# Optimization experiments

Measured on AMD Instinct MI355X. Metric: run time of the kernel, lower is better.

## Reference

```python
import jax, jax.numpy as jnp
import numpy as np

B, S, D, H = 2, 2048, 768, 12
HD = D // H


def setup_inputs() -> dict:
    key = jax.random.key(0)
    ks = jax.random.split(key, 6)
    x = jax.random.normal(ks[0], (B, S, D), dtype=jnp.float32)
    # causal mask: 1.0 where attention is disallowed (upper triangle), broadcast to [B,H,S,S]
    mask = (1.0 - jnp.tril(jnp.ones((S, S), dtype=jnp.float32)))[None, None]
    std = 0.02
    Wq = jax.random.normal(ks[1], (D, D), dtype=jnp.float32) * std
    Wk = jax.random.normal(ks[2], (D, D), dtype=jnp.float32) * std
    Wv = jax.random.normal(ks[3], (D, D), dtype=jnp.float32) * std
    Wo = jax.random.normal(ks[4], (D, D), dtype=jnp.float32) * (1.0 / np.sqrt(D))
    bq = jnp.zeros((D,), jnp.float32)
    bk = jnp.zeros((D,), jnp.float32)
    bv = jnp.zeros((D,), jnp.float32)
    bo = jnp.zeros((D,), jnp.float32)
    return {"x": x, "mask": mask, "Wq": Wq, "bq": bq, "Wk": Wk, "bk": bk,
            "Wv": Wv, "bv": bv, "Wo": Wo, "bo": bo}


def _split_heads(t):
    # [B,S,D] -> [B,H,S,hd]
    return t.reshape(B, S, H, HD).transpose(0, 2, 1, 3)


def reference(x, mask, Wq, bq, Wk, bk, Wv, bv, Wo, bo):
    q = _split_heads(x @ Wq + bq)
    k = _split_heads(x @ Wk + bk)
    v = _split_heads(x @ Wv + bv)
    scale = 1.0 / jnp.sqrt(jnp.asarray(HD, x.dtype))
    logits = jnp.einsum('bhqd,bhkd->bhqk', q, k) * scale  # [B,H,S,S]
    logits = logits + mask * (-1e9)
    attn = jax.nn.softmax(logits, axis=-1)
    ctx = jnp.einsum('bhqk,bhkd->bhqd', attn, v)          # [B,H,S,hd]
    ctx = ctx.transpose(0, 2, 1, 3).reshape(B, S, D)
    return ctx @ Wo + bo
```

## Files before the change

### kernel.cpp

```cpp
#include <hip/hip_runtime.h>
#include <math.h>

typedef unsigned short u16;
typedef unsigned int u32;
typedef unsigned long long u64;
typedef short bf16x8 __attribute__((ext_vector_type(8)));
typedef float f32x4 __attribute__((ext_vector_type(4)));
typedef float f32x16 __attribute__((ext_vector_type(16)));
typedef u32 u32x4 __attribute__((ext_vector_type(4)));

#define MFMA(a, b, c) __builtin_amdgcn_mfma_f32_16x16x32_bf16((a), (b), (c), 0, 0, 0)
#define MFMA32(a, b, c) __builtin_amdgcn_mfma_f32_32x32x16_bf16((a), (b), (c), 0, 0, 0)

#define BB 2
#define SS 2048
#define DD 768
#define HH 12
#define MROWS (BB * SS)
#define SCL 0.1803368801111244f

#if defined(__has_builtin)
#if __has_builtin(__builtin_amdgcn_global_load_lds)
#define HAS_GLL 1
#endif
#if __has_builtin(__builtin_amdgcn_exp2f)
#define HAS_EXP2 1
#endif
#endif
#ifndef HAS_GLL
#define HAS_GLL 0
#endif
#ifndef HAS_EXP2
#define HAS_EXP2 0
#endif

__device__ __forceinline__ float fexp2(float x) {
#if HAS_EXP2
  return __builtin_amdgcn_exp2f(x);
#else
  return exp2f(x);
#endif
}

__device__ __forceinline__ u16 f2bf(float f) {
  u32 u = __float_as_uint(f);
  u += 0x7FFFu + ((u >> 16) & 1u);
  return (u16)(u >> 16);
}
__device__ __forceinline__ float bf2f(u16 v) {
  return __uint_as_float(((u32)v) << 16);
}
__device__ __forceinline__ u32 cvtpk(float a, float b) {
  u32 r;
  asm("v_cvt_pk_bf16_f32 %0, %1, %2" : "=v"(r) : "v"(a), "v"(b));
  return r;
}

#if HAS_GLL
__device__ __forceinline__ void gload_lds16(const u16* g, u16* l) {
  __builtin_amdgcn_global_load_lds(
      (const __attribute__((address_space(1))) void*)(u64)(uintptr_t)g,
      (__attribute__((address_space(3))) void*)(u64)(uintptr_t)l, 16, 0, 0);
}
#endif

__global__ __launch_bounds__(256) void k_convert(const float* __restrict__ in,
                                                 u16* __restrict__ out, int n) {
  int i = (blockIdx.x * 256 + threadIdx.x) * 4;
  if (i < n) {
    float4 v = *(const float4*)(in + i);
    ushort4 o;
    o.x = f2bf(v.x); o.y = f2bf(v.y); o.z = f2bf(v.z); o.w = f2bf(v.w);
    *(ushort4*)(out + i) = o;
  }
}

__global__ __launch_bounds__(256) void k_transpose_w(
    const float* __restrict__ Wq, const float* __restrict__ Wk,
    const float* __restrict__ Wv, const float* __restrict__ Wo,
    u16* __restrict__ out) {
  const float* W = (blockIdx.z == 0) ? Wq : (blockIdx.z == 1) ? Wk
                   : (blockIdx.z == 2) ? Wv : Wo;
  u16* o = out + (size_t)blockIdx.z * DD * DD;
  __shared__ float tile[32][33];
  int kt = blockIdx.x * 32, nt = blockIdx.y * 32;
  int tx = threadIdx.x & 31, ty = threadIdx.x >> 5;
#pragma unroll
  for (int r = 0; r < 4; r++) {
    int row = ty + r * 8;
    tile[row][tx] = W[(size_t)(kt + row) * DD + nt + tx];
  }
  __syncthreads();
#pragma unroll
  for (int r = 0; r < 4; r++) {
    int row = ty + r * 8;
    o[(size_t)(nt + row) * DD + kt + tx] = f2bf(tile[tx][row]);
  }
}

template <bool OUT_BF16>
__device__ __forceinline__ void gemm128(const u16* __restrict__ A,
                                        const u16* __restrict__ Bt,
                                        const float* __restrict__ bias,
                                        void* __restrict__ Cout, int m0, int n0) {
  __shared__ __align__(16) u16 Al[128 * 32];
  __shared__ __align__(16) u16 Bl[128 * 32];
  int t = threadIdx.x;
  int lane = t & 63, w = t >> 6;
  int wm = (w >> 1) * 64, wn = (w & 1) * 64;
  int l15 = lane & 15, l4 = lane >> 4;
  f32x4 acc[4][4];
#pragma unroll
  for (int i = 0; i < 4; i++)
#pragma unroll
    for (int j = 0; j < 4; j++) acc[i][j] = (f32x4){0.f, 0.f, 0.f, 0.f};

#if HAS_GLL
  int srow = w * 32 + (lane >> 2);
  int skc = (lane & 3) * 8;
#endif

  for (int k0 = 0; k0 < DD; k0 += 32) {
#if HAS_GLL
#pragma unroll
    for (int rep = 0; rep < 2; rep++) {
      int row = srow + rep * 16;
      gload_lds16(A + (size_t)(m0 + row) * DD + k0 + skc,
                  &Al[(w * 32 + rep * 16) * 32]);
      gload_lds16(Bt + (size_t)(n0 + row) * DD + k0 + skc,
                  &Bl[(w * 32 + rep * 16) * 32]);
    }
#else
#pragma unroll
    for (int rep = 0; rep < 2; rep++) {
      int idx = rep * 256 + t;
      int row = idx >> 2, kc = (idx & 3) * 8;
      *(uint4*)&Al[row * 32 + kc] =
          *(const uint4*)(A + (size_t)(m0 + row) * DD + k0 + kc);
      *(uint4*)&Bl[row * 32 + kc] =
          *(const uint4*)(Bt + (size_t)(n0 + row) * DD + k0 + kc);
    }
#endif
    __syncthreads();
    bf16x8 af[4], bfr[4];
#pragma unroll
    for (int mb = 0; mb < 4; mb++)
      af[mb] = *(const bf16x8*)(&Al[(wm + mb * 16 + l15) * 32 + l4 * 8]);
#pragma unroll
    for (int nb = 0; nb < 4; nb++)
      bfr[nb] = *(const bf16x8*)(&Bl[(wn + nb * 16 + l15) * 32 + l4 * 8]);
#pragma unroll
    for (int mb = 0; mb < 4; mb++)
#pragma unroll
      for (int nb = 0; nb < 4; nb++)
        acc[mb][nb] = MFMA(af[mb], bfr[nb], acc[mb][nb]);
    __syncthreads();
  }
#pragma unroll
  for (int nb = 0; nb < 4; nb++) {
    int col = n0 + wn + nb * 16 + l15;
    float bs = bias[col];
#pragma unroll
    for (int mb = 0; mb < 4; mb++) {
#pragma unroll
      for (int r = 0; r < 4; r++) {
        int row = m0 + wm + mb * 16 + l4 * 4 + r;
        float vv = acc[mb][nb][r] + bs;
        if (OUT_BF16)
          ((u16*)Cout)[(size_t)row * DD + col] = f2bf(vv);
        else
          ((float*)Cout)[(size_t)row * DD + col] = vv;
      }
    }
  }
}

__global__ __launch_bounds__(256) void k_gemm_qkv(
    const u16* __restrict__ xb, const u16* __restrict__ Wt,
    const float* __restrict__ bq, const float* __restrict__ bk,
    const float* __restrict__ bv, u16* __restrict__ qkv) {
  int z = blockIdx.z;
  const u16* Bt = Wt + (size_t)z * DD * DD;
  const float* bias = (z == 0) ? bq : (z == 1) ? bk : bv;
  u16* out = qkv + (size_t)z * MROWS * DD;
  gemm128<true>(xb, Bt, bias, out, blockIdx.x * 128, blockIdx.y * 128);
}

__global__ __launch_bounds__(256) void k_gemm_out(
    const u16* __restrict__ ctx, const u16* __restrict__ Wot,
    const float* __restrict__ bo, float* __restrict__ out) {
  gemm128<false>(ctx, Wot, bo, out, blockIdx.x * 128, blockIdx.y * 128);
}

__global__ __launch_bounds__(256) void k_attn2(
    const u16* __restrict__ qb, const u16* __restrict__ kb,
    const u16* __restrict__ vb, u16* __restrict__ PO,
    float* __restrict__ PM, float* __restrict__ PL, u16* __restrict__ ctx,
    int CH2, int tot) {
  __shared__ __align__(16) u16 Vt[2][64 * 32];
  int bh = blockIdx.x;
  int s = tot - 1 - (int)blockIdx.y;
  int qt = 15, pre = 0;
#pragma unroll 16
  for (int q = 0; q < 16; q++) {
    int nq = (4 * (q + 1) + CH2 - 1) / CH2;
    if (s < pre + nq) { qt = q; break; }
    pre += nq;
  }
  int c = s - pre;
  int ntile = 4 * (qt + 1);
  int n = (ntile + CH2 - 1) / CH2;
  int len = (ntile - 1 - c) / n + 1;

  int b = bh / HH, h = bh % HH;
  int t = threadIdx.x, wq = t >> 6, lane = t & 63;
  int l31 = lane & 31, hi = lane >> 5;
  size_t rowbase = (size_t)b * SS;
  int hcol = h * 64;
  int qtq = qt * 128 + wq * 32;

  const u16* qp = qb + (rowbase + qtq + l31) * DD + hcol + hi * 8;
  bf16x8 qf0 = *(const bf16x8*)(qp);
  bf16x8 qf1 = *(const bf16x8*)(qp + 16);
  bf16x8 qf2 = *(const bf16x8*)(qp + 32);
  bf16x8 qf3 = *(const bf16x8*)(qp + 48);

  const u16* kbase = kb + rowbase * DD + hcol;
  const u16* vbase = vb + rowbase * DD + hcol;

  f32x16 o0, o1;
#pragma unroll
  for (int r = 0; r < 16; r++) { o0[r] = 0.f; o1[r] = 0.f; }
  float m_r = -3e38f, l_r = 0.f;

  int vk = t & 31, vd0 = (t >> 5) * 8;
  {
    uint4 v0 = *(const uint4*)(vbase + (size_t)(c * 32 + vk) * DD + vd0);
    u16 el[8];
    *(uint4*)el = v0;
    char* Vn = (char*)Vt[0];
#pragma unroll
    for (int ii = 0; ii < 8; ii++) {
      int d = vd0 + ii;
      *(u16*)(Vn + ((d * 64 + vk * 2) ^ (((d >> 1) & 3) << 4))) = el[ii];
    }
  }
  int dsw = ((l31 >> 1) & 3) << 4;

  for (int i = 0; i < len; i++) {
    int k32 = c + i * n;
    __syncthreads();
    uint4 vnext;
    if (i + 1 < len) {
      int nk = c + (i + 1) * n;
      vnext = *(const uint4*)(vbase + (size_t)(nk * 32 + vk) * DD + vd0);
    }
    bool act = (k32 * 32 <= qtq + 31);
    if (act) {
      const u16* kp = kbase + (size_t)(k32 * 32 + l31) * DD + hi * 8;
      bf16x8 kf0 = *(const bf16x8*)(kp);
      bf16x8 kf1 = *(const bf16x8*)(kp + 16);
      bf16x8 kf2 = *(const bf16x8*)(kp + 32);
      bf16x8 kf3 = *(const bf16x8*)(kp + 48);
      f32x16 sa;
#pragma unroll
      for (int r = 0; r < 16; r++) sa[r] = 0.f;
      __builtin_amdgcn_s_setprio(1);
      sa = MFMA32(kf0, qf0, sa);
      sa = MFMA32(kf1, qf1, sa);
      sa = MFMA32(kf2, qf2, sa);
      sa = MFMA32(kf3, qf3, sa);
      __builtin_amdgcn_s_setprio(0);
      float p[16];
#pragma unroll
      for (int r = 0; r < 16; r++) p[r] = sa[r] * SCL;
      if (k32 * 32 + 31 > qtq) {
        int qg = qtq + l31;
#pragma unroll
        for (int r = 0; r < 16; r++) {
          int kg = k32 * 32 + (r & 3) + 8 * (r >> 2) + 4 * hi;
          p[r] = (kg > qg) ? -1e30f : p[r];
        }
      }
      float mx = p[0];
#pragma unroll
      for (int r = 1; r < 16; r++) mx = fmaxf(mx, p[r]);
      mx = fmaxf(mx, __shfl_xor(mx, 32, 64));
      float mn = fmaxf(m_r, mx);
      float al = fexp2(m_r - mn);
      m_r = mn;
      float rs = 0.f;
#pragma unroll
      for (int r = 0; r < 16; r++) {
        p[r] = fexp2(p[r] - mn);
        rs += p[r];
      }
      rs += __shfl_xor(rs, 32, 64);
      l_r = l_r * al + rs;
      u32 cc0 = cvtpk(p[0], p[1]), cc1 = cvtpk(p[2], p[3]);
      u32 cc2 = cvtpk(p[4], p[5]), cc3 = cvtpk(p[6], p[7]);
      u32 cc4 = cvtpk(p[8], p[9]), cc5 = cvtpk(p[10], p[11]);
      u32 cc6 = cvtpk(p[12], p[13]), cc7 = cvtpk(p[14], p[15]);
      u32 xx0 = __shfl_xor(cc0, 32, 64), xx1 = __shfl_xor(cc1, 32, 64);
      u32 xx2 = __shfl_xor(cc2, 32, 64), xx3 = __shfl_xor(cc3, 32, 64);
      u32 xx4 = __shfl_xor(cc4, 32, 64), xx5 = __shfl_xor(cc5, 32, 64);
      u32 xx6 = __shfl_xor(cc6, 32, 64), xx7 = __shfl_xor(cc7, 32, 64);
      u32x4 P0 = {hi ? xx2 : cc0, hi ? xx3 : cc1, hi ? cc2 : xx0, hi ? cc3 : xx1};
      u32x4 P1 = {hi ? xx6 : cc4, hi ? xx7 : cc5, hi ? cc6 : xx4, hi ? cc7 : xx5};
      bf16x8 pb0 = __builtin_bit_cast(bf16x8, P0);
      bf16x8 pb1 = __builtin_bit_cast(bf16x8, P1);
#pragma unroll
      for (int r = 0; r < 16; r++) { o0[r] *= al; o1[r] *= al; }
      const char* Vc = (const char*)Vt[i & 1];
      bf16x8 a00 = *(const bf16x8*)(Vc + ((l31 * 64 + hi * 16) ^ dsw));
      bf16x8 a01 = *(const bf16x8*)(Vc + ((l31 * 64 + 32 + hi * 16) ^ dsw));
      bf16x8 a10 = *(const bf16x8*)(Vc + (((32 + l31) * 64 + hi * 16) ^ dsw));
      bf16x8 a11 = *(const bf16x8*)(Vc + (((32 + l31) * 64 + 32 + hi * 16) ^ dsw));
      __builtin_amdgcn_s_setprio(1);
      o0 = MFMA32(a00, pb0, o0);
      o0 = MFMA32(a01, pb1, o0);
      o1 = MFMA32(a10, pb0, o1);
      o1 = MFMA32(a11, pb1, o1);
      __builtin_amdgcn_s_setprio(0);
    }
    if (i + 1 < len) {
      u16 el[8];
      *(uint4*)el = vnext;
      char* Vn = (char*)Vt[(i + 1) & 1];
#pragma unroll
      for (int ii = 0; ii < 8; ii++) {
        int d = vd0 + ii;
        *(u16*)(Vn + ((d * 64 + vk * 2) ^ (((d >> 1) & 3) << 4))) = el[ii];
      }
    }
  }
  float inv = 1.f / l_r;
  ushort4 g[8];
#pragma unroll
  for (int rq = 0; rq < 4; rq++) {
    g[rq].x = f2bf(o0[rq * 4 + 0] * inv);
    g[rq].y = f2bf(o0[rq * 4 + 1] * inv);
    g[rq].z = f2bf(o0[rq * 4 + 2] * inv);
    g[rq].w = f2bf(o0[rq * 4 + 3] * inv);
    g[4 + rq].x = f2bf(o1[rq * 4 + 0] * inv);
    g[4 + rq].y = f2bf(o1[rq * 4 + 1] * inv);
    g[4 + rq].z = f2bf(o1[rq * 4 + 2] * inv);
    g[4 + rq].w = f2bf(o1[rq * 4 + 3] * inv);
  }
  if (n == 1) {
    u16* dst = ctx + (rowbase + qtq + l31) * DD + hcol;
#pragma unroll
    for (int db = 0; db < 2; db++)
#pragma unroll
      for (int rq = 0; rq < 4; rq++)
        *(ushort4*)(dst + db * 32 + rq * 8 + hi * 4) = g[db * 4 + rq];
  } else {
    size_t gs = (size_t)bh * tot + pre + c;
    u16* po = PO + gs * 8192 + (size_t)(wq * 32 + l31) * 64;
#pragma unroll
    for (int db = 0; db < 2; db++)
#pragma unroll
      for (int rq = 0; rq < 4; rq++)
        *(ushort4*)(po + db * 32 + rq * 8 + hi * 4) = g[db * 4 + rq];
    if (hi == 0) {
      PM[gs * 128 + wq * 32 + l31] = m_r;
      PL[gs * 128 + wq * 32 + l31] = l_r;
    }
  }
}

__global__ __launch_bounds__(256) void k_combine2(
    const u16* __restrict__ PO, const float* __restrict__ PM,
    const float* __restrict__ PL, u16* __restrict__ ctx, int CH2, int tot,
    int qt0) {
  int bh = blockIdx.x, qt = qt0 + blockIdx.y;
  int b = bh / HH, h = bh % HH;
  int ntile = 4 * (qt + 1);
  int n = (ntile + CH2 - 1) / CH2;
  int pre = 0;
#pragma unroll 16
  for (int q = 0; q < 16; q++)
    if (q < qt) pre += (4 * (q + 1) + CH2 - 1) / CH2;
  size_t base = (size_t)bh * tot + pre;
  int t = threadIdx.x;
  int ql = t >> 1, d0 = (t & 1) * 32;
  float w[8];
  float M = -3e38f;
#pragma unroll 8
  for (int i = 0; i < 8; i++) {
    if (i < n) {
      float mi = PM[(base + i) * 128 + ql];
      w[i] = mi;
      M = fmaxf(M, mi);
    }
  }
  float L = 0.f;
#pragma unroll 8
  for (int i = 0; i < 8; i++) {
    if (i < n) {
      float wi = PL[(base + i) * 128 + ql] * fexp2(w[i] - M);
      w[i] = wi;
      L += wi;
    }
  }
  float inv = 1.f / L;
  float acc[32];
#pragma unroll
  for (int j = 0; j < 32; j++) acc[j] = 0.f;
#pragma unroll 8
  for (int i = 0; i < 8; i++) {
    if (i < n) {
      float wi = w[i] * inv;
      const u16* p = PO + (base + i) * 8192 + (size_t)ql * 64 + d0;
#pragma unroll
      for (int q8 = 0; q8 < 4; q8++) {
        bf16x8 v = *(const bf16x8*)(p + q8 * 8);
#pragma unroll
        for (int j = 0; j < 8; j++) acc[q8 * 8 + j] += wi * bf2f((u16)v[j]);
      }
    }
  }
  u16 ob[32];
#pragma unroll
  for (int j = 0; j < 32; j++) ob[j] = f2bf(acc[j]);
  u16* dst = ctx + ((size_t)b * SS + qt * 128 + ql) * DD + h * 64 + d0;
#pragma unroll
  for (int q8 = 0; q8 < 4; q8++)
    *(uint4*)(dst + q8 * 8) = *(uint4*)(ob + q8 * 8);
}

extern "C" void kernel_launch(void* const* d_in, const int* in_sizes, int n_in,
                              void* d_out, int out_size, void* d_ws, size_t ws_size,
                              hipStream_t stream) {
  const float* x  = (const float*)d_in[0];
  const float* Wq = (const float*)d_in[2];
  const float* bq = (const float*)d_in[3];
  const float* Wk = (const float*)d_in[4];
  const float* bk = (const float*)d_in[5];
  const float* Wv = (const float*)d_in[6];
  const float* bv = (const float*)d_in[7];
  const float* Wo = (const float*)d_in[8];
  const float* bo = (const float*)d_in[9];
  float* out = (float*)d_out;

  char* ws = (char*)d_ws;
  const size_t XN = (size_t)MROWS * DD;
  const size_t WN = (size_t)DD * DD;
  u16* xb  = (u16*)ws;
  u16* Wt  = (u16*)(ws + XN * 2);
  u16* qkv = (u16*)(ws + XN * 2 + WN * 8);
  u16* ctx = (u16*)(ws + XN * 2 + WN * 8 + XN * 6);
  const size_t base = XN * 2 + WN * 8 + XN * 6 + XN * 2;

  int CH2 = 64, tot = 0;
  {
    const int cands[4] = {8, 16, 32, 64};
    for (int ci = 0; ci < 4; ci++) {
      int ch = cands[ci];
      int tt = 0;
      for (int q = 0; q < 16; q++) tt += (4 * (q + 1) + ch - 1) / ch;
      size_t need = base + (size_t)24 * tt * 8192 * 2 +
                    2 * (size_t)24 * tt * 128 * 4;
      if (ws_size >= need) { CH2 = ch; tot = tt; break; }
      if (ci == 3) { CH2 = ch; tot = tt; }
    }
  }
  const size_t NCHUNK = (size_t)24 * tot;
  u16*   PO = (u16*)(ws + base);
  float* PM = (float*)(ws + base + NCHUNK * 8192 * 2);
  float* PL = PM + NCHUNK * 128;
  int qt0 = CH2 / 4;

  k_convert<<<dim3((int)(XN / 1024)), 256, 0, stream>>>(x, xb, (int)XN);
  k_transpose_w<<<dim3(24, 24, 4), 256, 0, stream>>>(Wq, Wk, Wv, Wo, Wt);
  k_gemm_qkv<<<dim3(32, 6, 3), 256, 0, stream>>>(xb, Wt, bq, bk, bv, qkv);
  k_attn2<<<dim3(24, tot), 256, 0, stream>>>(qkv, qkv + XN, qkv + 2 * XN, PO, PM,
                                             PL, ctx, CH2, tot);
  if (qt0 < 16)
    k_combine2<<<dim3(24, 16 - qt0), 256, 0, stream>>>(PO, PM, PL, ctx, CH2, tot,
                                                       qt0);
  k_gemm_out<<<dim3(32, 6), 256, 0, stream>>>(ctx, Wt + 3 * WN, bo, out);
}
```

Baseline: 121.6 us.

## Prefetch K tiles, skip lazy softmax rescales, and allow finer KV split

Moves the K fragment loads for the next key tile ahead of the current tile's compute, so global load latency overlaps with the MFMA and softmax work. Adds a lazy-rescale rule: the running max and the output accumulators are only rescaled when the new tile max exceeds the old one by more than a threshold, wave-wide. It also uses a tree max reduction, and adds a split size of 4 tiles as the first choice for the KV split, with the combine kernel widened to handle up to 16 partials. Risks are higher register pressure, possible fp overflow from the threshold if it is set badly, and extra combine traffic from the finer split.

New measurement: 150.1 us. 23.5% more time.

```diff
diff --git a/kernel.cpp b/kernel.cpp
--- a/kernel.cpp
+++ b/kernel.cpp
@@ -18,6 +18,8 @@
 #define HH 12
 #define MROWS (BB * SS)
 #define SCL 0.1803368801111244f
+#define THR 8.0f
+
 
 #if defined(__has_builtin)
 #if __has_builtin(__builtin_amdgcn_global_load_lds)
@@ -245,23 +247,29 @@
       *(u16*)(Vn + ((d * 64 + vk * 2) ^ (((d >> 1) & 3) << 4))) = el[ii];
     }
   }
+  const u16* kp0 = kbase + (size_t)(c * 32 + l31) * DD + hi * 8;
+  bf16x8 kf0 = *(const bf16x8*)(kp0);
+  bf16x8 kf1 = *(const bf16x8*)(kp0 + 16);
+  bf16x8 kf2 = *(const bf16x8*)(kp0 + 32);
+  bf16x8 kf3 = *(const bf16x8*)(kp0 + 48);
   int dsw = ((l31 >> 1) & 3) << 4;
 
   for (int i = 0; i < len; i++) {
     int k32 = c + i * n;
     __syncthreads();
     uint4 vnext;
+    bf16x8 kn0, kn1, kn2, kn3;
     if (i + 1 < len) {
       int nk = c + (i + 1) * n;
       vnext = *(const uint4*)(vbase + (size_t)(nk * 32 + vk) * DD + vd0);
+      const u16* kp = kbase + (size_t)(nk * 32 + l31) * DD + hi * 8;
+      kn0 = *(const bf16x8*)(kp);
+      kn1 = *(const bf16x8*)(kp + 16);
+      kn2 = *(const bf16x8*)(kp + 32);
+      kn3 = *(const bf16x8*)(kp + 48);
     }
     bool act = (k32 * 32 <= qtq + 31);
     if (act) {
-      const u16* kp = kbase + (size_t)(k32 * 32 + l31) * DD + hi * 8;
-      bf16x8 kf0 = *(const bf16x8*)(kp);
-      bf16x8 kf1 = *(const bf16x8*)(kp + 16);
-      bf16x8 kf2 = *(const bf16x8*)(kp + 32);
-      bf16x8 kf3 = *(const bf16x8*)(kp + 48);
       f32x16 sa;
 #pragma unroll
       for (int r = 0; r < 16; r++) sa[r] = 0.f;
@@ -282,21 +290,29 @@
           p[r] = (kg > qg) ? -1e30f : p[r];
         }
       }
-      float mx = p[0];
-#pragma unroll
-      for (int r = 1; r < 16; r++) mx = fmaxf(mx, p[r]);
+      float mx01 = fmaxf(p[0], p[1]), mx23 = fmaxf(p[2], p[3]);
+      float mx45 = fmaxf(p[4], p[5]), mx67 = fmaxf(p[6], p[7]);
+      float mx89 = fmaxf(p[8], p[9]), mxab = fmaxf(p[10], p[11]);
+      float mxcd = fmaxf(p[12], p[13]), mxef = fmaxf(p[14], p[15]);
+      float mx = fmaxf(fmaxf(fmaxf(mx01, mx23), fmaxf(mx45, mx67)),
+                       fmaxf(fmaxf(mx89, mxab), fmaxf(mxcd, mxef)));
       mx = fmaxf(mx, __shfl_xor(mx, 32, 64));
-      float mn = fmaxf(m_r, mx);
-      float al = fexp2(m_r - mn);
-      m_r = mn;
+      if (!__all(mx - m_r <= THR)) {
+        float mn = fmaxf(m_r, mx);
+        float al = fexp2(m_r - mn);
+        m_r = mn;
+        l_r *= al;
+#pragma unroll
+        for (int r = 0; r < 16; r++) { o0[r] *= al; o1[r] *= al; }
+      }
       float rs = 0.f;
 #pragma unroll
       for (int r = 0; r < 16; r++) {
-        p[r] = fexp2(p[r] - mn);
+        p[r] = fexp2(p[r] - m_r);
         rs += p[r];
       }
       rs += __shfl_xor(rs, 32, 64);
-      l_r = l_r * al + rs;
+      l_r += rs;
       u32 cc0 = cvtpk(p[0], p[1]), cc1 = cvtpk(p[2], p[3]);
       u32 cc2 = cvtpk(p[4], p[5]), cc3 = cvtpk(p[6], p[7]);
       u32 cc4 = cvtpk(p[8], p[9]), cc5 = cvtpk(p[10], p[11]);
@@ -309,8 +325,6 @@
       u32x4 P1 = {hi ? xx6 : cc4, hi ? xx7 : cc5, hi ? cc6 : xx4, hi ? cc7 : xx5};
       bf16x8 pb0 = __builtin_bit_cast(bf16x8, P0);
       bf16x8 pb1 = __builtin_bit_cast(bf16x8, P1);
-#pragma unroll
-      for (int r = 0; r < 16; r++) { o0[r] *= al; o1[r] *= al; }
       const char* Vc = (const char*)Vt[i & 1];
       bf16x8 a00 = *(const bf16x8*)(Vc + ((l31 * 64 + hi * 16) ^ dsw));
       bf16x8 a01 = *(const bf16x8*)(Vc + ((l31 * 64 + 32 + hi * 16) ^ dsw));
@@ -324,6 +338,7 @@
       __builtin_amdgcn_s_setprio(0);
     }
     if (i + 1 < len) {
+      kf0 = kn0; kf1 = kn1; kf2 = kn2; kf3 = kn3;
       u16 el[8];
       *(uint4*)el = vnext;
       char* Vn = (char*)Vt[(i + 1) & 1];
@@ -384,10 +399,10 @@
   size_t base = (size_t)bh * tot + pre;
   int t = threadIdx.x;
   int ql = t >> 1, d0 = (t & 1) * 32;
-  float w[8];
+  float w[16];
   float M = -3e38f;
-#pragma unroll 8
-  for (int i = 0; i < 8; i++) {
+#pragma unroll 16
+  for (int i = 0; i < 16; i++) {
     if (i < n) {
       float mi = PM[(base + i) * 128 + ql];
       w[i] = mi;
@@ -395,8 +410,8 @@
     }
   }
   float L = 0.f;
-#pragma unroll 8
-  for (int i = 0; i < 8; i++) {
+#pragma unroll 16
+  for (int i = 0; i < 16; i++) {
     if (i < n) {
       float wi = PL[(base + i) * 128 + ql] * fexp2(w[i] - M);
       w[i] = wi;
@@ -407,8 +422,8 @@
   float acc[32];
 #pragma unroll
   for (int j = 0; j < 32; j++) acc[j] = 0.f;
-#pragma unroll 8
-  for (int i = 0; i < 8; i++) {
+#pragma unroll 16
+  for (int i = 0; i < 16; i++) {
     if (i < n) {
       float wi = w[i] * inv;
       const u16* p = PO + (base + i) * 8192 + (size_t)ql * 64 + d0;
@@ -454,15 +469,15 @@
 
   int CH2 = 64, tot = 0;
   {
-    const int cands[4] = {8, 16, 32, 64};
-    for (int ci = 0; ci < 4; ci++) {
+    const int cands[5] = {4, 8, 16, 32, 64};
+    for (int ci = 0; ci < 5; ci++) {
       int ch = cands[ci];
       int tt = 0;
       for (int q = 0; q < 16; q++) tt += (4 * (q + 1) + ch - 1) / ch;
       size_t need = base + (size_t)24 * tt * 8192 * 2 +
                     2 * (size_t)24 * tt * 128 * 4;
       if (ws_size >= need) { CH2 = ch; tot = tt; break; }
-      if (ci == 3) { CH2 = ch; tot = tt; }
+      if (ci == 4) { CH2 = ch; tot = tt; }
     }
   }
   const size_t NCHUNK = (size_t)24 * tot;
```

## Halve attention query tile to 64 rows with 128-thread blocks

Applied to the files above, without the earlier changes.

Shrinks the attention query tile from 128 to 64 rows, using 2 waves per block instead of 4. That doubles the number of query tiles and split-K chunks. Each thread now stages two V slices into LDS, and the partial-output and combine layouts are resized to match. The aim is finer-grained work and better load balance across CUs for causal attention. The cost is that each K/V tile is reused by fewer query rows, so global K/V traffic rises. The row-max reduction is also rewritten as a tree.

After: 125.2 us. +3.0%, slower.

```diff
diff --git a/kernel.cpp b/kernel.cpp
--- a/kernel.cpp
+++ b/kernel.cpp
@@ -18,6 +18,7 @@
 #define HH 12
 #define MROWS (BB * SS)
 #define SCL 0.1803368801111244f
+
 
 #if defined(__has_builtin)
 #if __has_builtin(__builtin_amdgcn_global_load_lds)
@@ -192,7 +193,7 @@
   gemm128<false>(ctx, Wot, bo, out, blockIdx.x * 128, blockIdx.y * 128);
 }
 
-__global__ __launch_bounds__(256) void k_attn2(
+__global__ __launch_bounds__(128) void k_attn2(
     const u16* __restrict__ qb, const u16* __restrict__ kb,
     const u16* __restrict__ vb, u16* __restrict__ PO,
     float* __restrict__ PM, float* __restrict__ PL, u16* __restrict__ ctx,
@@ -200,15 +201,15 @@
   __shared__ __align__(16) u16 Vt[2][64 * 32];
   int bh = blockIdx.x;
   int s = tot - 1 - (int)blockIdx.y;
-  int qt = 15, pre = 0;
-#pragma unroll 16
-  for (int q = 0; q < 16; q++) {
-    int nq = (4 * (q + 1) + CH2 - 1) / CH2;
+  int qt = 31, pre = 0;
+#pragma unroll 32
+  for (int q = 0; q < 32; q++) {
+    int nq = (2 * (q + 1) + CH2 - 1) / CH2;
     if (s < pre + nq) { qt = q; break; }
     pre += nq;
   }
   int c = s - pre;
-  int ntile = 4 * (qt + 1);
+  int ntile = 2 * (qt + 1);
   int n = (ntile + CH2 - 1) / CH2;
   int len = (ntile - 1 - c) / n + 1;
 
@@ -217,7 +218,7 @@
   int l31 = lane & 31, hi = lane >> 5;
   size_t rowbase = (size_t)b * SS;
   int hcol = h * 64;
-  int qtq = qt * 128 + wq * 32;
+  int qtq = qt * 64 + wq * 32;
 
   const u16* qp = qb + (rowbase + qtq + l31) * DD + hcol + hi * 8;
   bf16x8 qf0 = *(const bf16x8*)(qp);
@@ -233,16 +234,20 @@
   for (int r = 0; r < 16; r++) { o0[r] = 0.f; o1[r] = 0.f; }
   float m_r = -3e38f, l_r = 0.f;
 
-  int vk = t & 31, vd0 = (t >> 5) * 8;
+  int vk = t & 31, vd0 = ((t >> 5) & 3) * 8;
   {
-    uint4 v0 = *(const uint4*)(vbase + (size_t)(c * 32 + vk) * DD + vd0);
-    u16 el[8];
-    *(uint4*)el = v0;
     char* Vn = (char*)Vt[0];
 #pragma unroll
-    for (int ii = 0; ii < 8; ii++) {
-      int d = vd0 + ii;
-      *(u16*)(Vn + ((d * 64 + vk * 2) ^ (((d >> 1) & 3) << 4))) = el[ii];
+    for (int rep = 0; rep < 2; rep++) {
+      int d8 = vd0 + rep * 32;
+      uint4 v0 = *(const uint4*)(vbase + (size_t)(c * 32 + vk) * DD + d8);
+      u16 el[8];
+      *(uint4*)el = v0;
+#pragma unroll
+      for (int ii = 0; ii < 8; ii++) {
+        int d = d8 + ii;
+        *(u16*)(Vn + ((d * 64 + vk * 2) ^ (((d >> 1) & 3) << 4))) = el[ii];
+      }
     }
   }
   int dsw = ((l31 >> 1) & 3) << 4;
@@ -250,10 +255,13 @@
   for (int i = 0; i < len; i++) {
     int k32 = c + i * n;
     __syncthreads();
-    uint4 vnext;
+    uint4 vnext[2];
     if (i + 1 < len) {
       int nk = c + (i + 1) * n;
-      vnext = *(const uint4*)(vbase + (size_t)(nk * 32 + vk) * DD + vd0);
+#pragma unroll
+      for (int rep = 0; rep < 2; rep++)
+        vnext[rep] =
+            *(const uint4*)(vbase + (size_t)(nk * 32 + vk) * DD + vd0 + rep * 32);
     }
     bool act = (k32 * 32 <= qtq + 31);
     if (act) {
@@ -282,9 +290,12 @@
           p[r] = (kg > qg) ? -1e30f : p[r];
         }
       }
-      float mx = p[0];
-#pragma unroll
-      for (int r = 1; r < 16; r++) mx = fmaxf(mx, p[r]);
+      float mx01 = fmaxf(p[0], p[1]), mx23 = fmaxf(p[2], p[3]);
+      float mx45 = fmaxf(p[4], p[5]), mx67 = fmaxf(p[6], p[7]);
+      float mx89 = fmaxf(p[8], p[9]), mxab = fmaxf(p[10], p[11]);
+      float mxcd = fmaxf(p[12], p[13]), mxef = fmaxf(p[14], p[15]);
+      float mx = fmaxf(fmaxf(fmaxf(mx01, mx23), fmaxf(mx45, mx67)),
+                       fmaxf(fmaxf(mx89, mxab), fmaxf(mxcd, mxef)));
       mx = fmaxf(mx, __shfl_xor(mx, 32, 64));
       float mn = fmaxf(m_r, mx);
       float al = fexp2(m_r - mn);
@@ -324,13 +335,16 @@
       __builtin_amdgcn_s_setprio(0);
     }
     if (i + 1 < len) {
-      u16 el[8];
-      *(uint4*)el = vnext;
       char* Vn = (char*)Vt[(i + 1) & 1];
 #pragma unroll
-      for (int ii = 0; ii < 8; ii++) {
-        int d = vd0 + ii;
-        *(u16*)(Vn + ((d * 64 + vk * 2) ^ (((d >> 1) & 3) << 4))) = el[ii];
+      for (int rep = 0; rep < 2; rep++) {
+        u16 el[8];
+        *(uint4*)el = vnext[rep];
+#pragma unroll
+        for (int ii = 0; ii < 8; ii++) {
+          int d = vd0 + rep * 32 + ii;
+          *(u16*)(Vn + ((d * 64 + vk * 2) ^ (((d >> 1) & 3) << 4))) = el[ii];
+        }
       }
     }
   }
@@ -356,15 +370,15 @@
         *(ushort4*)(dst + db * 32 + rq * 8 + hi * 4) = g[db * 4 + rq];
   } else {
     size_t gs = (size_t)bh * tot + pre + c;
-    u16* po = PO + gs * 8192 + (size_t)(wq * 32 + l31) * 64;
+    u16* po = PO + gs * 4096 + (size_t)(wq * 32 + l31) * 64;
 #pragma unroll
     for (int db = 0; db < 2; db++)
 #pragma unroll
       for (int rq = 0; rq < 4; rq++)
         *(ushort4*)(po + db * 32 + rq * 8 + hi * 4) = g[db * 4 + rq];
     if (hi == 0) {
-      PM[gs * 128 + wq * 32 + l31] = m_r;
-      PL[gs * 128 + wq * 32 + l31] = l_r;
+      PM[gs * 64 + wq * 32 + l31] = m_r;
+      PL[gs * 64 + wq * 32 + l31] = l_r;
     }
   }
 }
@@ -375,21 +389,21 @@
     int qt0) {
   int bh = blockIdx.x, qt = qt0 + blockIdx.y;
   int b = bh / HH, h = bh % HH;
-  int ntile = 4 * (qt + 1);
+  int ntile = 2 * (qt + 1);
   int n = (ntile + CH2 - 1) / CH2;
   int pre = 0;
-#pragma unroll 16
-  for (int q = 0; q < 16; q++)
-    if (q < qt) pre += (4 * (q + 1) + CH2 - 1) / CH2;
+#pragma unroll 32
+  for (int q = 0; q < 32; q++)
+    if (q < qt) pre += (2 * (q + 1) + CH2 - 1) / CH2;
   size_t base = (size_t)bh * tot + pre;
   int t = threadIdx.x;
-  int ql = t >> 1, d0 = (t & 1) * 32;
+  int ql = t >> 2, cs = (t & 3) << 4;
   float w[8];
   float M = -3e38f;
 #pragma unroll 8
   for (int i = 0; i < 8; i++) {
     if (i < n) {
-      float mi = PM[(base + i) * 128 + ql];
+      float mi = PM[(base + i) * 64 + ql];
       w[i] = mi;
       M = fmaxf(M, mi);
     }
@@ -398,35 +412,35 @@
 #pragma unroll 8
   for (int i = 0; i < 8; i++) {
     if (i < n) {
-      float wi = PL[(base + i) * 128 + ql] * fexp2(w[i] - M);
+      float wi = PL[(base + i) * 64 + ql] * fexp2(w[i] - M);
       w[i] = wi;
       L += wi;
     }
   }
   float inv = 1.f / L;
-  float acc[32];
-#pragma unroll
-  for (int j = 0; j < 32; j++) acc[j] = 0.f;
+  float acc[16];
+#pragma unroll
+  for (int j = 0; j < 16; j++) acc[j] = 0.f;
 #pragma unroll 8
   for (int i = 0; i < 8; i++) {
     if (i < n) {
       float wi = w[i] * inv;
-      const u16* p = PO + (base + i) * 8192 + (size_t)ql * 64 + d0;
-#pragma unroll
-      for (int q8 = 0; q8 < 4; q8++) {
-        bf16x8 v = *(const bf16x8*)(p + q8 * 8);
-#pragma unroll
-        for (int j = 0; j < 8; j++) acc[q8 * 8 + j] += wi * bf2f((u16)v[j]);
-      }
-    }
-  }
-  u16 ob[32];
-#pragma unroll
-  for (int j = 0; j < 32; j++) ob[j] = f2bf(acc[j]);
-  u16* dst = ctx + ((size_t)b * SS + qt * 128 + ql) * DD + h * 64 + d0;
-#pragma unroll
-  for (int q8 = 0; q8 < 4; q8++)
-    *(uint4*)(dst + q8 * 8) = *(uint4*)(ob + q8 * 8);
+      const u16* p = PO + (base + i) * 4096 + (size_t)ql * 64 + cs;
+      bf16x8 v0 = *(const bf16x8*)p;
+      bf16x8 v1 = *(const bf16x8*)(p + 8);
+#pragma unroll
+      for (int j = 0; j < 8; j++) {
+        acc[j]     += wi * bf2f((u16)v0[j]);
+        acc[8 + j] += wi * bf2f((u16)v1[j]);
+      }
+    }
+  }
+  u16 ob[16];
+#pragma unroll
+  for (int j = 0; j < 16; j++) ob[j] = f2bf(acc[j]);
+  u16* dst = ctx + ((size_t)b * SS + qt * 64 + ql) * DD + h * 64 + cs;
+  *(uint4*)dst = *(uint4*)ob;
+  *(uint4*)(dst + 8) = *(uint4*)(ob + 8);
 }
 
 extern "C" void kernel_launch(void* const* d_in, const int* in_sizes, int n_in,
@@ -458,26 +472,26 @@
     for (int ci = 0; ci < 4; ci++) {
       int ch = cands[ci];
       int tt = 0;
-      for (int q = 0; q < 16; q++) tt += (4 * (q + 1) + ch - 1) / ch;
-      size_t need = base + (size_t)24 * tt * 8192 * 2 +
-                    2 * (size_t)24 * tt * 128 * 4;
+      for (int q = 0; q < 32; q++) tt += (2 * (q + 1) + ch - 1) / ch;
+      size_t need = base + (size_t)24 * tt * 4096 * 2 +
+                    2 * (size_t)24 * tt * 64 * 4;
       if (ws_size >= need) { CH2 = ch; tot = tt; break; }
       if (ci == 3) { CH2 = ch; tot = tt; }
     }
   }
   const size_t NCHUNK = (size_t)24 * tot;
   u16*   PO = (u16*)(ws + base);
-  float* PM = (float*)(ws + base + NCHUNK * 8192 * 2);
-  float* PL = PM + NCHUNK * 128;
-  int qt0 = CH2 / 4;
+  float* PM = (float*)(ws + base + NCHUNK * 4096 * 2);
+  float* PL = PM + NCHUNK * 64;
+  int qt0 = CH2 / 2;
 
   k_convert<<<dim3((int)(XN / 1024)), 256, 0, stream>>>(x, xb, (int)XN);
   k_transpose_w<<<dim3(24, 24, 4), 256, 0, stream>>>(Wq, Wk, Wv, Wo, Wt);
   k_gemm_qkv<<<dim3(32, 6, 3), 256, 0, stream>>>(xb, Wt, bq, bk, bv, qkv);
-  k_attn2<<<dim3(24, tot), 256, 0, stream>>>(qkv, qkv + XN, qkv + 2 * XN, PO, PM,
+  k_attn2<<<dim3(24, tot), 128, 0, stream>>>(qkv, qkv + XN, qkv + 2 * XN, PO, PM,
                                              PL, ctx, CH2, tot);
-  if (qt0 < 16)
-    k_combine2<<<dim3(24, 16 - qt0), 256, 0, stream>>>(PO, PM, PL, ctx, CH2, tot,
+  if (qt0 < 32)
+    k_combine2<<<dim3(24, 32 - qt0), 256, 0, stream>>>(PO, PM, PL, ctx, CH2, tot,
                                                        qt0);
   k_gemm_out<<<dim3(32, 6), 256, 0, stream>>>(ctx, Wt + 3 * WN, bo, out);
 }
```
